# Optimization experiments

Measured on AMD Instinct MI355X. Metric: run time of the kernel, lower is better.

## Reference

```python
import jax, jax.numpy as jnp
import numpy as np

LP, LQ, B, D, H = 500, 64, 64, 256, 150  # lp, lq, batch_size, in_size, hidden_size*2


def setup_inputs() -> dict:
    key = jax.random.key(0)
    ks = jax.random.split(key, 12)
    s = 0.05
    f32 = jnp.float32
    return {
        "Up": jax.random.normal(ks[0], (LP, B, D), f32),
        "Uq": jax.random.normal(ks[1], (LQ, B, D), f32),
        "Wp": jax.random.normal(ks[2], (H, 2 * D), f32) * s,
        "Wq": jax.random.normal(ks[3], (H, 2 * D), f32) * s,
        "Wv": jax.random.normal(ks[4], (H, H), f32) * s,
        "Wg": jax.random.normal(ks[5], (4 * D, 4 * D), f32) * s,
        "V": jax.random.normal(ks[6], (B, H), f32),        # per-batch attention vector (squeezed [B,H,1])
        "v0": jax.random.normal(ks[7], (B, H), f32),       # initial GRU state self.v
        "W_ih": jax.random.normal(ks[8], (3 * H, 2 * D), f32) * s,
        "W_hh": jax.random.normal(ks[9], (3 * H, H), f32) * s,
        "b_ih": jax.random.normal(ks[10], (3 * H,), f32) * s,
        "b_hh": jax.random.normal(ks[11], (3 * H,), f32) * s,
    }


def reference(Up, Uq, Wp, Wq, Wv, Wg, V, v0, W_ih, W_hh, b_ih, b_hh):
    Din = Up.shape[2]
    # torch.cat([U, U[arange]], dim=2) == duplicate features
    Up2 = jnp.concatenate([Up, Up], axis=2)  # [lp, B, 2D]
    Uq2 = jnp.concatenate([Uq, Uq], axis=2)  # [lq, B, 2D]
    # Wq(Uq2) is loop-invariant in the original loop; hoist it (same math)
    Wuq = jnp.einsum('qbd,hd->qbh', Uq2, Wq)  # [lq, B, H]

    def gru_cell(x, h):
        gi = x @ W_ih.T + b_ih  # [B, 3H]
        gh = h @ W_hh.T + b_hh
        i_r, i_z, i_n = jnp.split(gi, 3, axis=1)
        h_r, h_z, h_n = jnp.split(gh, 3, axis=1)
        r = jax.nn.sigmoid(i_r + h_r)
        z = jax.nn.sigmoid(i_z + h_z)
        n = jnp.tanh(i_n + r * h_n)
        return (1.0 - z) * n + z * h

    def step(v, up_i):  # up_i: [B, 2D], v: [B, H]
        Wup = up_i @ Wp.T                                   # [B, H]
        x = jnp.tanh(Wup[None] + Wuq + (v @ Wv.T)[None])    # [lq, B, H]
        s = jnp.einsum('qbh,bh->bq', x, V)                  # bmm(x^T, V).squeeze
        a = jax.nn.softmax(s, axis=1)                       # [B, lq]
        c = jnp.einsum('bq,qbd->bd', a, Uq2)                # [B, 2D]
        r = jnp.concatenate([up_i, c], axis=1)              # [B, 4D]
        g = jax.nn.sigmoid(r @ Wg.T)
        r = g * r
        c_ = r[:, 2 * Din:]                                 # gated context -> GRU input
        v_new = gru_cell(c_, v)
        return v_new, v_new

    _, vs = jax.lax.scan(step, v0, Up2)  # [lp, B, H]
    # dropout is identity in eval mode
    return vs
```

## Files before the change

kernel.cpp:

```cpp
#include <hip/hip_runtime.h>
#include <hip/hip_fp16.h>

#define LP 500

typedef _Float16 h2f __attribute__((ext_vector_type(2)));
typedef _Float16 h8f __attribute__((ext_vector_type(8)));

constexpr size_t OFF_WVH2 = 0;
constexpr size_t OFF_WGF2 = 46208;
constexpr size_t OFF_WIH2 = 111744;
constexpr size_t OFF_WPF  = 227456;
constexpr size_t OFF_WQF  = 265856;
constexpr size_t OFF_WUQ  = 304256;
constexpr size_t OFF_P1   = 918656;
constexpr size_t OFF_WG1  = OFF_P1;
constexpr size_t OFF_GUH  = 5718656;
constexpr size_t OFF_UPT  = 13910656;
constexpr size_t OFF_M2   = OFF_UPT;
constexpr size_t OFF_UQT  = 22102656;
constexpr size_t OFF_UQT2 = OFF_UQT;
constexpr size_t WS_FLOATS = 23151232;

__device__ __forceinline__ float fast_rcp(float x) { return __builtin_amdgcn_rcpf(x); }
__device__ __forceinline__ float sigm(float x)   { return fast_rcp(1.f + __expf(-x)); }
__device__ __forceinline__ float tanh_f(float x) { return 1.f - 2.f * fast_rcp(1.f + __expf(2.f * x)); }

__global__ __launch_bounds__(256) void k_prep(const float* __restrict__ Wp, const float* __restrict__ Wq,
                                              const float* __restrict__ Wg, const float* __restrict__ Wv,
                                              const float* __restrict__ Whh, const float* __restrict__ Wih,
                                              float* __restrict__ ws) {
    int i = blockIdx.x * 256 + threadIdx.x;
    if (i < 46208) {
        int k2 = i / 608, m = i - k2 * 608;
        float lo = 0.f, hi = 0.f;
        if (k2 < 75 && m < 600) {
            if (m < 150) { lo = Wv[m * 150 + 2 * k2]; hi = Wv[m * 150 + 2 * k2 + 1]; }
            else { int mm = m - 150; lo = Whh[mm * 150 + 2 * k2]; hi = Whh[mm * 150 + 2 * k2 + 1]; }
        }
        ((h2f*)(ws + OFF_WVH2))[i] = h2f{(_Float16)lo, (_Float16)hi};
        return;
    }
    i -= 46208;
    if (i < 65536) {
        int k2 = i >> 9, j = i & 511;
        int d = 2 * k2;
        size_t r = (size_t)(512 + j) * 1024;
        float lo = Wg[r + 512 + d] + Wg[r + 768 + d];
        float hi = Wg[r + 512 + d + 1] + Wg[r + 768 + d + 1];
        ((h2f*)(ws + OFF_WGF2))[i] = h2f{(_Float16)lo, (_Float16)hi};
        return;
    }
    i -= 65536;
    if (i < 115712) {
        int k2 = i / 452, m = i - k2 * 452;
        float lo = 0.f, hi = 0.f;
        if (m < 450) { lo = Wih[m * 512 + 2 * k2]; hi = Wih[m * 512 + 2 * k2 + 1]; }
        ((h2f*)(ws + OFF_WIH2))[i] = h2f{(_Float16)lo, (_Float16)hi};
        return;
    }
    i -= 115712;
    if (i < 38400) { int h = i >> 8, d = i & 255; ws[OFF_WPF + i] = Wp[h * 512 + d] + Wp[h * 512 + 256 + d]; return; }
    i -= 38400;
    if (i < 38400) { int h = i >> 8, d = i & 255; ws[OFF_WQF + i] = Wq[h * 512 + d] + Wq[h * 512 + 256 + d]; return; }
    i -= 38400;
    if (i < 131072) { int j = i >> 8, d = i & 255; size_t r = (size_t)(512 + j) * 1024; ws[OFF_WG1 + i] = Wg[r + d] + Wg[r + 256 + d]; return; }
}

__global__ __launch_bounds__(256) void k_tr(const float* __restrict__ X, float* __restrict__ XT) {
    __shared__ float tile[64][65];
    size_t base = (size_t)blockIdx.x * 16384;
    for (int ph = 0; ph < 4; ++ph) {
        for (int i = threadIdx.x; i < 4096; i += 256) {
            int b = i >> 6, dl = i & 63;
            tile[b][dl] = X[base + (size_t)b * 256 + ph * 64 + dl];
        }
        __syncthreads();
        for (int i = threadIdx.x; i < 4096; i += 256) {
            int d = i >> 6, bl = i & 63;
            XT[base + (size_t)(ph * 64 + d) * 64 + bl] = tile[bl][d];
        }
        __syncthreads();
    }
}

__global__ __launch_bounds__(256) void k_gemm(const float* __restrict__ XT, const float* __restrict__ Wf,
                                              float* __restrict__ outF, _Float16* __restrict__ outH,
                                              int Hrows, int tilesPerT) {
    __shared__ float OL[64 * 33];
    int bidx = blockIdx.x;
    int t = bidx / tilesPerT, tile = bidx - t * tilesPerT;
    int w = threadIdx.x >> 6, lane = threadIdx.x & 63;
    int h0 = __builtin_amdgcn_readfirstlane(tile * 32 + w * 8);
    const float* x = XT + (size_t)t * 16384;
    float acc[8];
    const float* wr[8];
#pragma unroll
    for (int r = 0; r < 8; ++r) {
        int hr = h0 + r; if (hr >= Hrows) hr = Hrows - 1;
        wr[r] = Wf + (size_t)hr * 256;
        acc[r] = 0.f;
    }
    for (int d = 0; d < 256; d += 4) {
        float cv0 = x[(d + 0) * 64 + lane];
        float cv1 = x[(d + 1) * 64 + lane];
        float cv2 = x[(d + 2) * 64 + lane];
        float cv3 = x[(d + 3) * 64 + lane];
#pragma unroll
        for (int r = 0; r < 8; ++r) {
            float4 wv = *(const float4*)(wr[r] + d);
            acc[r] += cv0 * wv.x + cv1 * wv.y + cv2 * wv.z + cv3 * wv.w;
        }
    }
#pragma unroll
    for (int r = 0; r < 8; ++r) { int hl = w * 8 + r; OL[lane * 33 + hl] = acc[r]; }
    __syncthreads();
    int hbase = tile * 32;
    int nh = Hrows - hbase; if (nh > 32) nh = 32;
    for (int i = threadIdx.x; i < 64 * nh; i += 256) {
        int b = i / nh, hl = i - b * nh;
        float val = OL[b * 33 + hl];
        size_t idx = (size_t)t * 64 * Hrows + (size_t)b * Hrows + hbase + hl;
        if (outF) outF[idx] = val;
        else outH[idx] = (_Float16)val;
    }
}

__global__ __launch_bounds__(256) void k_uqt(const float* __restrict__ Uq, h2f* __restrict__ UqT2) {
    int b = blockIdx.x, d = threadIdx.x;
    for (int q2 = 0; q2 < 32; ++q2) {
        float lo = Uq[(size_t)(2 * q2) * 16384 + b * 256 + d];
        float hi = Uq[(size_t)(2 * q2 + 1) * 16384 + b * 256 + d];
        UqT2[(size_t)b * 8192 + q2 * 256 + d] = h2f{(_Float16)lo, (_Float16)hi};
    }
}

__global__ __launch_bounds__(512) void k_mgemm(const float* __restrict__ Uq,
                                               const float* ws_ro,
                                               h2f* M2) {
    __shared__ _Float16 uqf[64 * 256];
    int b = blockIdx.x, j = threadIdx.x;
    const h2f* Wgf2 = (const h2f*)(ws_ro + OFF_WGF2);
    for (int u = threadIdx.x; u < 16384; u += 512) {
        int q = u >> 8, d = u & 255;
        uqf[u] = (_Float16)Uq[(size_t)q * 16384 + b * 256 + d];
    }
    __syncthreads();
    for (int qc = 0; qc < 8; ++qc) {
        float acc[8];
#pragma unroll
        for (int i = 0; i < 8; ++i) acc[i] = 0.f;
        for (int k2 = 0; k2 < 128; ++k2) {
            h2f w = Wgf2[k2 * 512 + j];
            float wlo = (float)w[0], whi = (float)w[1];
#pragma unroll
            for (int i = 0; i < 8; ++i) {
                acc[i] += (float)uqf[(qc * 8 + i) * 256 + 2 * k2] * wlo
                        + (float)uqf[(qc * 8 + i) * 256 + 2 * k2 + 1] * whi;
            }
        }
#pragma unroll
        for (int p = 0; p < 4; ++p)
            M2[(size_t)b * 16384 + (size_t)(qc * 4 + p) * 512 + j] =
                h2f{(_Float16)acc[2 * p], (_Float16)acc[2 * p + 1]};
    }
}

__global__ __launch_bounds__(768, 3) void k_scan16(
    const float* __restrict__ V, const float* __restrict__ v0,
    const float* __restrict__ bih, const float* __restrict__ bhh,
    const float* __restrict__ ws, float* __restrict__ out) {
    __shared__ __attribute__((aligned(16))) float red[3072];
    __shared__ __attribute__((aligned(16))) _Float16 vh[152];
    __shared__ float pbf[152];
    __shared__ float ghf[452];
    __shared__ float Vb[152];
    __shared__ float bihL[452];
    __shared__ float bhhL[452];
    __shared__ float vf[152];
    __shared__ float sa[64];
    __shared__ __attribute__((aligned(8))) h2f sah[32];
    __shared__ __attribute__((aligned(8))) h2f c_p[256];
    __shared__ __attribute__((aligned(16))) h2f uql[8192];
    __shared__ __attribute__((aligned(16))) h2f m2l[16384];
    __shared__ __attribute__((aligned(16))) h2f wihl[18 * 452];

    const int tid = threadIdx.x, b = blockIdx.x;
    const int lane = tid & 63;
    const h2f* Wvh2 = (const h2f*)(ws + OFF_WVH2);
    const h2f* Wih2 = (const h2f*)(ws + OFF_WIH2);
    const h2f* UqT2b = (const h2f*)(ws + OFF_UQT2) + (size_t)b * 8192;
    const h2f* M2b = (const h2f*)(ws + OFF_M2) + (size_t)b * 16384;
    const float* WuqG = ws + OFF_WUQ;
    const float* P1 = ws + OFF_P1;
    const _Float16* GuH = (const _Float16*)(ws + OFF_GUH);

    const int p1_ks = tid / 152, p1_mq = tid - p1_ks * 152;
    const h2f* wv_base = Wvh2 + (size_t)(p1_ks * 15) * 608 + 4 * p1_mq;
    const int p4_ks = tid / 113, p4_mq = tid - p4_ks * 113;
    const h2f* wih_base = Wih2 + (size_t)(p4_ks * 44) * 452 + 4 * p4_mq;

    const int w12 = tid >> 6;
    const int nq = (w12 < 4) ? 6 : 5;
    const int q0 = (w12 < 4) ? w12 * 6 : 24 + (w12 - 4) * 5;
    _Float16 wq[18];
#pragma unroll
    for (int i = 0; i < 6; ++i)
#pragma unroll
        for (int it = 0; it < 3; ++it) {
            int idx = lane + 64 * it;
            wq[i * 3 + it] = (_Float16)((i < nq && idx < 150) ? WuqG[(size_t)(q0 + i) * 9600 + b * 150 + idx] : 0.f);
        }

    h8f wihr[12];
#pragma unroll
    for (int i = 0; i < 12; ++i)
        wihr[i] = (tid < 678) ? *(const h8f*)(wih_base + (size_t)(3 + i) * 452) : h8f{};

    {
        const h8f* su = (const h8f*)UqT2b;
        h8f* du = (h8f*)uql;
        for (int u = tid; u < 2048; u += 768) du[u] = su[u];
        const h8f* sm = (const h8f*)M2b;
        h8f* dm = (h8f*)m2l;
        for (int u = tid; u < 4096; u += 768) dm[u] = sm[u];
        h8f* dw = (h8f*)wihl;
        for (int u = tid; u < 2034; u += 768) {
            int slot = u / 113, off = u - slot * 113;
            int ks = slot / 3, i = slot - ks * 3;
            dw[u] = *(const h8f*)(Wih2 + (size_t)(ks * 44 + i) * 452 + off * 4);
        }
    }

    for (int i = tid; i < 150; i += 768) { Vb[i] = V[b * 150 + i]; float v = v0[b * 150 + i]; vf[i] = v; vh[i] = (_Float16)v; }
    for (int i = tid; i < 450; i += 768) { bihL[i] = bih[i]; bhhL[i] = bhh[i]; }
    if (tid < 2) vh[150 + tid] = (_Float16)0.f;
    __syncthreads();

    for (int t = 0; t < LP; ++t) {
        float p1v = 0.f;
        if (tid < 150) p1v = P1[(size_t)t * 9600 + b * 150 + tid];
        float guv = 0.f;
        if (tid < 512) guv = (float)GuH[(size_t)t * 32768 + b * 512 + tid];

        if (tid < 760) {
            const h2f* vh2 = (const h2f*)vh;
            float a0 = 0.f, a1 = 0.f, a2 = 0.f, a3 = 0.f;
#pragma unroll 5
            for (int i = 0; i < 15; ++i) {
                h8f w = *(const h8f*)(wv_base + (size_t)i * 608);
                h2f x = vh2[p1_ks * 15 + i];
                a0 = __builtin_amdgcn_fdot2(h2f{w[0], w[1]}, x, a0, false);
                a1 = __builtin_amdgcn_fdot2(h2f{w[2], w[3]}, x, a1, false);
                a2 = __builtin_amdgcn_fdot2(h2f{w[4], w[5]}, x, a2, false);
                a3 = __builtin_amdgcn_fdot2(h2f{w[6], w[7]}, x, a3, false);
            }
            *(float4*)(red + p1_ks * 608 + 4 * p1_mq) = float4{a0, a1, a2, a3};
        }
        __syncthreads();
        if (tid < 150) {
            float s = red[tid] + red[608 + tid] + red[1216 + tid] + red[1824 + tid] + red[2432 + tid];
            pbf[tid] = s + p1v;
        }
        __syncthreads();
        {
#pragma unroll
            for (int i = 0; i < 6; ++i) {
                if (i < nq) {
                    float part = 0.f;
#pragma unroll
                    for (int it = 0; it < 3; ++it) {
                        int idx = lane + 64 * it;
                        if (idx < 150)
                            part += tanh_f(pbf[idx] + (float)wq[i * 3 + it]) * Vb[idx];
                    }
                    part += __shfl_xor(part, 32); part += __shfl_xor(part, 16);
                    part += __shfl_xor(part, 8);  part += __shfl_xor(part, 4);
                    part += __shfl_xor(part, 2);  part += __shfl_xor(part, 1);
                    if (lane == 0) sa[q0 + i] = part;
                }
            }
        }
        __syncthreads();
        if (tid < 64) {
            float s = sa[tid];
            float m = s;
            m = fmaxf(m, __shfl_xor(m, 32)); m = fmaxf(m, __shfl_xor(m, 16));
            m = fmaxf(m, __shfl_xor(m, 8));  m = fmaxf(m, __shfl_xor(m, 4));
            m = fmaxf(m, __shfl_xor(m, 2));  m = fmaxf(m, __shfl_xor(m, 1));
            float e = __expf(s - m);
            float su = e;
            su += __shfl_xor(su, 32); su += __shfl_xor(su, 16); su += __shfl_xor(su, 8);
            su += __shfl_xor(su, 4);  su += __shfl_xor(su, 2);  su += __shfl_xor(su, 1);
            float a = e * fast_rcp(su);
            float an = __shfl_xor(a, 1);
            if ((tid & 1) == 0) sah[tid >> 1] = h2f{(_Float16)a, (_Float16)an};
        } else if (tid < 514) {
            int m = 86 + tid;
            ghf[m - 150] = red[m] + red[608 + m] + red[1216 + m] + red[1824 + m] + red[2432 + m] + bhhL[m - 150];
        }
        __syncthreads();
        if (tid < 256) {
            int cks = tid >> 6, cqd = tid & 63;
            float a0 = 0.f, a1 = 0.f, a2 = 0.f, a3 = 0.f;
#pragma unroll
            for (int i = 0; i < 8; ++i) {
                int q2 = cks * 8 + i;
                h8f u = *(const h8f*)(uql + q2 * 256 + 4 * cqd);
                h2f ap = sah[q2];
                a0 = __builtin_amdgcn_fdot2(h2f{u[0], u[1]}, ap, a0, false);
                a1 = __builtin_amdgcn_fdot2(h2f{u[2], u[3]}, ap, a1, false);
                a2 = __builtin_amdgcn_fdot2(h2f{u[4], u[5]}, ap, a2, false);
                a3 = __builtin_amdgcn_fdot2(h2f{u[6], u[7]}, ap, a3, false);
            }
            *(float4*)(red + cks * 256 + 4 * cqd) = float4{a0, a1, a2, a3};
        } else {
            int gt = tid - 256, gks = gt >> 7, gjq = gt & 127;
            float a0 = 0.f, a1 = 0.f, a2 = 0.f, a3 = 0.f;
#pragma unroll
            for (int i = 0; i < 8; ++i) {
                int q2 = gks * 8 + i;
                h8f m8 = *(const h8f*)(m2l + q2 * 512 + 4 * gjq);
                h2f ap = sah[q2];
                a0 = __builtin_amdgcn_fdot2(h2f{m8[0], m8[1]}, ap, a0, false);
                a1 = __builtin_amdgcn_fdot2(h2f{m8[2], m8[3]}, ap, a1, false);
                a2 = __builtin_amdgcn_fdot2(h2f{m8[4], m8[5]}, ap, a2, false);
                a3 = __builtin_amdgcn_fdot2(h2f{m8[6], m8[7]}, ap, a3, false);
            }
            *(float4*)(red + 1024 + gks * 512 + 4 * gjq) = float4{a0, a1, a2, a3};
        }
        __syncthreads();
        if (tid < 512) {
            float g = guv + red[1024 + tid] + red[1536 + tid] + red[2048 + tid] + red[2560 + tid];
            int dd = tid & 255;
            float cc = red[dd] + red[256 + dd] + red[512 + dd] + red[768 + dd];
            float val = sigm(g) * cc;
            float vn2 = __shfl_xor(val, 1);
            if ((tid & 1) == 0) c_p[tid >> 1] = h2f{(_Float16)val, (_Float16)vn2};
        }
        __syncthreads();
        if (tid < 678) {
            float a0 = 0.f, a1 = 0.f, a2 = 0.f, a3 = 0.f;
#pragma unroll
            for (int i = 0; i < 3; ++i) {
                h8f w = *(const h8f*)(wihl + (size_t)(p4_ks * 3 + i) * 452 + 4 * p4_mq);
                h2f cp = c_p[p4_ks * 44 + i];
                a0 = __builtin_amdgcn_fdot2(h2f{w[0], w[1]}, cp, a0, false);
                a1 = __builtin_amdgcn_fdot2(h2f{w[2], w[3]}, cp, a1, false);
                a2 = __builtin_amdgcn_fdot2(h2f{w[4], w[5]}, cp, a2, false);
                a3 = __builtin_amdgcn_fdot2(h2f{w[6], w[7]}, cp, a3, false);
            }
#pragma unroll
            for (int i = 3; i < 15; ++i) {
                h8f w = wihr[i - 3];
                h2f cp = c_p[p4_ks * 44 + i];
                a0 = __builtin_amdgcn_fdot2(h2f{w[0], w[1]}, cp, a0, false);
                a1 = __builtin_amdgcn_fdot2(h2f{w[2], w[3]}, cp, a1, false);
                a2 = __builtin_amdgcn_fdot2(h2f{w[4], w[5]}, cp, a2, false);
                a3 = __builtin_amdgcn_fdot2(h2f{w[6], w[7]}, cp, a3, false);
            }
#pragma unroll 15
            for (int i = 15; i < 44; ++i) {
                int row = p4_ks * 44 + i;
                if (row < 256) {
                    h8f w = *(const h8f*)(wih_base + (size_t)i * 452);
                    h2f cp = c_p[row];
                    a0 = __builtin_amdgcn_fdot2(h2f{w[0], w[1]}, cp, a0, false);
                    a1 = __builtin_amdgcn_fdot2(h2f{w[2], w[3]}, cp, a1, false);
                    a2 = __builtin_amdgcn_fdot2(h2f{w[4], w[5]}, cp, a2, false);
                    a3 = __builtin_amdgcn_fdot2(h2f{w[6], w[7]}, cp, a3, false);
                }
            }
            *(float4*)(red + p4_ks * 456 + 4 * p4_mq) = float4{a0, a1, a2, a3};
        }
        __syncthreads();
        if (tid < 150) {
            float gi0 = red[tid] + red[456 + tid] + red[912 + tid] + red[1368 + tid] + red[1824 + tid] + red[2280 + tid];
            int m1 = 150 + tid;
            float gi1 = red[m1] + red[456 + m1] + red[912 + m1] + red[1368 + m1] + red[1824 + m1] + red[2280 + m1];
            int m2 = 300 + tid;
            float gi2 = red[m2] + red[456 + m2] + red[912 + m2] + red[1368 + m2] + red[1824 + m2] + red[2280 + m2];
            float r = sigm(gi0 + bihL[tid] + ghf[tid]);
            float z = sigm(gi1 + bihL[150 + tid] + ghf[150 + tid]);
            float n = tanh_f(gi2 + bihL[300 + tid] + r * ghf[300 + tid]);
            float vn = (1.f - z) * n + z * vf[tid];
            vf[tid] = vn;
            vh[tid] = (_Float16)vn;
            out[(size_t)t * 9600 + b * 150 + tid] = vn;
        }
        __syncthreads();
    }
}

extern "C" void kernel_launch(void* const* d_in, const int* in_sizes, int n_in,
                              void* d_out, int out_size, void* d_ws, size_t ws_size,
                              hipStream_t stream) {
    const float* Up  = (const float*)d_in[0];
    const float* Uq  = (const float*)d_in[1];
    const float* Wp  = (const float*)d_in[2];
    const float* Wq  = (const float*)d_in[3];
    const float* Wv  = (const float*)d_in[4];
    const float* Wg  = (const float*)d_in[5];
    const float* V   = (const float*)d_in[6];
    const float* v0  = (const float*)d_in[7];
    const float* Wih = (const float*)d_in[8];
    const float* Whh = (const float*)d_in[9];
    const float* bih = (const float*)d_in[10];
    const float* bhh = (const float*)d_in[11];
    float* out = (float*)d_out;
    float* ws = (float*)d_ws;

    if (ws_size < WS_FLOATS * sizeof(float)) return;

    k_prep<<<1701, 256, 0, stream>>>(Wp, Wq, Wg, Wv, Whh, Wih, ws);
    k_tr<<<500, 256, 0, stream>>>(Up, ws + OFF_UPT);
    k_tr<<<64, 256, 0, stream>>>(Uq, ws + OFF_UQT);
    k_gemm<<<8000, 256, 0, stream>>>(ws + OFF_UPT, ws + OFF_WG1, nullptr, (_Float16*)(ws + OFF_GUH), 512, 16);
    k_gemm<<<2500, 256, 0, stream>>>(ws + OFF_UPT, ws + OFF_WPF, ws + OFF_P1, nullptr, 150, 5);
    k_gemm<<<320, 256, 0, stream>>>(ws + OFF_UQT, ws + OFF_WQF, ws + OFF_WUQ, nullptr, 150, 5);
    k_uqt<<<64, 256, 0, stream>>>(Uq, (h2f*)(ws + OFF_UQT2));
    k_mgemm<<<64, 512, 0, stream>>>(Uq, ws, (h2f*)(ws + OFF_M2));
    k_scan16<<<64, 768, 0, stream>>>(V, v0, bih, bhh, ws, out);
}
```

Baseline: 5.604 ms.

## Split Wv/Whh matvec so hidden-gate part overlaps attention scoring

The fused per-step matvec over the concatenated Wv/W_hh weights is split. Only the 152 columns needed for the attention bias (Wv plus two gate columns) are computed before the first barrier, using a 20-way K-split. The remaining hidden-gate columns are computed by the spare waves 8-11 concurrently with the tanh/score phase, which now uses 8 waves of 8 queries each. This shortens the serial critical path per scan step, at the cost of more reduction partials and unequal work across waves.

```diff
diff --git a/kernel.cpp b/kernel.cpp
--- a/kernel.cpp
+++ b/kernel.cpp
@@ -165,7 +165,7 @@
     }
 }
 
-__global__ __launch_bounds__(768, 3) void k_scan16(
+__global__ __launch_bounds__(768, 3) void k_scan17(
     const float* __restrict__ V, const float* __restrict__ v0,
     const float* __restrict__ bih, const float* __restrict__ bhh,
     const float* __restrict__ ws, float* __restrict__ out) {
@@ -194,21 +194,21 @@
     const float* P1 = ws + OFF_P1;
     const _Float16* GuH = (const _Float16*)(ws + OFF_GUH);
 
-    const int p1_ks = tid / 152, p1_mq = tid - p1_ks * 152;
-    const h2f* wv_base = Wvh2 + (size_t)(p1_ks * 15) * 608 + 4 * p1_mq;
+    const int pA_g = tid / 38, pA_mq = tid - pA_g * 38;
+    const int pA_cnt = (pA_g < 16) ? 4 : 3;
+    const int pA_r0 = (pA_g < 16) ? pA_g * 4 : 64 + (pA_g - 16) * 3;
+    const h2f* pbw_base = Wvh2 + (size_t)pA_r0 * 608 + 4 * pA_mq;
     const int p4_ks = tid / 113, p4_mq = tid - p4_ks * 113;
     const h2f* wih_base = Wih2 + (size_t)(p4_ks * 44) * 452 + 4 * p4_mq;
 
     const int w12 = tid >> 6;
-    const int nq = (w12 < 4) ? 6 : 5;
-    const int q0 = (w12 < 4) ? w12 * 6 : 24 + (w12 - 4) * 5;
-    _Float16 wq[18];
-#pragma unroll
-    for (int i = 0; i < 6; ++i)
+    _Float16 wq[24];
+#pragma unroll
+    for (int i = 0; i < 8; ++i)
 #pragma unroll
         for (int it = 0; it < 3; ++it) {
             int idx = lane + 64 * it;
-            wq[i * 3 + it] = (_Float16)((i < nq && idx < 150) ? WuqG[(size_t)(q0 + i) * 9600 + b * 150 + idx] : 0.f);
+            wq[i * 3 + it] = (_Float16)((w12 < 8 && idx < 150) ? WuqG[(size_t)(w12 * 8 + i) * 9600 + b * 150 + idx] : 0.f);
         }
 
     h8f wihr[12];
@@ -245,39 +245,61 @@
         if (tid < 760) {
             const h2f* vh2 = (const h2f*)vh;
             float a0 = 0.f, a1 = 0.f, a2 = 0.f, a3 = 0.f;
-#pragma unroll 5
-            for (int i = 0; i < 15; ++i) {
-                h8f w = *(const h8f*)(wv_base + (size_t)i * 608);
-                h2f x = vh2[p1_ks * 15 + i];
-                a0 = __builtin_amdgcn_fdot2(h2f{w[0], w[1]}, x, a0, false);
-                a1 = __builtin_amdgcn_fdot2(h2f{w[2], w[3]}, x, a1, false);
-                a2 = __builtin_amdgcn_fdot2(h2f{w[4], w[5]}, x, a2, false);
-                a3 = __builtin_amdgcn_fdot2(h2f{w[6], w[7]}, x, a3, false);
-            }
-            *(float4*)(red + p1_ks * 608 + 4 * p1_mq) = float4{a0, a1, a2, a3};
-        }
-        __syncthreads();
-        if (tid < 150) {
-            float s = red[tid] + red[608 + tid] + red[1216 + tid] + red[1824 + tid] + red[2432 + tid];
-            pbf[tid] = s + p1v;
-        }
-        __syncthreads();
-        {
-#pragma unroll
-            for (int i = 0; i < 6; ++i) {
-                if (i < nq) {
-                    float part = 0.f;
-#pragma unroll
-                    for (int it = 0; it < 3; ++it) {
-                        int idx = lane + 64 * it;
-                        if (idx < 150)
-                            part += tanh_f(pbf[idx] + (float)wq[i * 3 + it]) * Vb[idx];
-                    }
-                    part += __shfl_xor(part, 32); part += __shfl_xor(part, 16);
-                    part += __shfl_xor(part, 8);  part += __shfl_xor(part, 4);
-                    part += __shfl_xor(part, 2);  part += __shfl_xor(part, 1);
-                    if (lane == 0) sa[q0 + i] = part;
+#pragma unroll
+            for (int i = 0; i < 4; ++i) {
+                if (i < pA_cnt) {
+                    h8f w = *(const h8f*)(pbw_base + (size_t)i * 608);
+                    h2f x = vh2[pA_r0 + i];
+                    a0 = __builtin_amdgcn_fdot2(h2f{w[0], w[1]}, x, a0, false);
+                    a1 = __builtin_amdgcn_fdot2(h2f{w[2], w[3]}, x, a1, false);
+                    a2 = __builtin_amdgcn_fdot2(h2f{w[4], w[5]}, x, a2, false);
+                    a3 = __builtin_amdgcn_fdot2(h2f{w[6], w[7]}, x, a3, false);
                 }
+            }
+            *(float4*)(red + pA_g * 152 + 4 * pA_mq) = float4{a0, a1, a2, a3};
+        }
+        __syncthreads();
+        if (tid < 152) {
+            float s = 0.f;
+#pragma unroll
+            for (int g = 0; g < 20; ++g) s += red[g * 152 + tid];
+            if (tid < 150) pbf[tid] = s + p1v;
+            else ghf[tid - 150] = s + bhhL[tid - 150];
+        }
+        __syncthreads();
+        if (w12 < 8) {
+#pragma unroll
+            for (int i = 0; i < 8; ++i) {
+                int q = w12 * 8 + i;
+                float part = 0.f;
+#pragma unroll
+                for (int it = 0; it < 3; ++it) {
+                    int idx = lane + 64 * it;
+                    if (idx < 150)
+                        part += tanh_f(pbf[idx] + (float)wq[i * 3 + it]) * Vb[idx];
+                }
+                part += __shfl_xor(part, 32); part += __shfl_xor(part, 16);
+                part += __shfl_xor(part, 8);  part += __shfl_xor(part, 4);
+                part += __shfl_xor(part, 2);  part += __shfl_xor(part, 1);
+                if (lane == 0) sa[q] = part;
+            }
+        } else {
+            int u = tid - 512;
+            if (u < 224) {
+                int ks = u / 112, mq = u - ks * 112;
+                const h2f* ghw = Wvh2 + (size_t)(ks * 38) * 608 + 4 * (38 + mq);
+                const h2f* vh2 = (const h2f*)vh;
+                float a0 = 0.f, a1 = 0.f, a2 = 0.f, a3 = 0.f;
+#pragma unroll 19
+                for (int r = 0; r < 38; ++r) {
+                    h8f w = *(const h8f*)(ghw + (size_t)r * 608);
+                    h2f x = vh2[ks * 38 + r];
+                    a0 = __builtin_amdgcn_fdot2(h2f{w[0], w[1]}, x, a0, false);
+                    a1 = __builtin_amdgcn_fdot2(h2f{w[2], w[3]}, x, a1, false);
+                    a2 = __builtin_amdgcn_fdot2(h2f{w[4], w[5]}, x, a2, false);
+                    a3 = __builtin_amdgcn_fdot2(h2f{w[6], w[7]}, x, a3, false);
+                }
+                *(float4*)(red + 2048 + ks * 448 + 4 * mq) = float4{a0, a1, a2, a3};
             }
         }
         __syncthreads();
@@ -294,9 +316,9 @@
             float a = e * fast_rcp(su);
             float an = __shfl_xor(a, 1);
             if ((tid & 1) == 0) sah[tid >> 1] = h2f{(_Float16)a, (_Float16)an};
-        } else if (tid < 514) {
-            int m = 86 + tid;
-            ghf[m - 150] = red[m] + red[608 + m] + red[1216 + m] + red[1824 + m] + red[2432 + m] + bhhL[m - 150];
+        } else if (tid < 512) {
+            int u = tid - 64;
+            ghf[2 + u] = red[2048 + u] + red[2048 + 448 + u] + bhhL[2 + u];
         }
         __syncthreads();
         if (tid < 256) {
@@ -419,5 +441,5 @@
     k_gemm<<<320, 256, 0, stream>>>(ws + OFF_UQT, ws + OFF_WQF, ws + OFF_WUQ, nullptr, 150, 5);
     k_uqt<<<64, 256, 0, stream>>>(Uq, (h2f*)(ws + OFF_UQT2));
     k_mgemm<<<64, 512, 0, stream>>>(Uq, ws, (h2f*)(ws + OFF_M2));
-    k_scan16<<<64, 768, 0, stream>>>(V, v0, bih, bhh, ws, out);
-}
+    k_scan17<<<64, 768, 0, stream>>>(V, v0, bih, bhh, ws, out);
+}
```

Result: slower. 6.525 ms (+16.4%).
